# Optimization experiments

Hardware: AMD Instinct MI355X
Metric: run time of the kernel (lower is better)

## Reference

```python
import jax, jax.numpy as jnp
import numpy as np
from jax import lax

# ---- static config (ProposalLayer config object) ----
BASE_SIZE = 16
RATIOS = np.array([0.5, 1.0, 2.0])
SCALES = np.array([8.0, 16.0, 32.0])
STRIDE = 16
PRE_NMS_TOPN = 6000
POST_NMS_TOPN = 300
MIN_THRESHOLD = 16.0
NMS_THRESH = 0.7
IMG_W = 4096
IMG_H = 2048
NEG_INF = jnp.float32(-1e30)


def _generate_anchors(base_size, ratios, scales):
    w = h = float(base_size)
    x_ctr = y_ctr = 0.5 * (base_size - 1)
    size = w * h
    size_ratios = size / ratios
    ws = np.round(np.sqrt(size_ratios))          # (R,)
    hs = np.round(ws * ratios)                   # (R,)
    ws = (ws[:, None] * scales[None, :]).ravel() # (R*S,)
    hs = (hs[:, None] * scales[None, :]).ravel()
    anchors = np.stack([x_ctr - 0.5 * (ws - 1), y_ctr - 0.5 * (hs - 1),
                        x_ctr + 0.5 * (ws - 1), y_ctr + 0.5 * (hs - 1)], axis=1)
    return anchors.astype(np.float32)            # (A, 4) in x1,y1,x2,y2


def _all_anchors(height, width, stride):
    anchors = _generate_anchors(BASE_SIZE, RATIOS, SCALES)      # (A,4)
    sx = np.arange(width) * stride
    sy = np.arange(height) * stride
    mx, my = np.meshgrid(sx, sy)                                # (H,W) each
    shifts = np.stack([mx.ravel(), my.ravel(), mx.ravel(), my.ravel()], axis=1)
    shifts = shifts.reshape(-1, 1, 4).astype(np.float32)        # (K,1,4), K iterates h-major
    return (anchors[None] + shifts).reshape(-1, 4)              # (K*A, 4)


def _decode(deltas, anchors):
    # deltas: (B, N, 4); anchors: (N, 4) -> boxes (B, N, 4)
    aw = anchors[:, 2] - anchors[:, 0] + 1.0
    ah = anchors[:, 3] - anchors[:, 1] + 1.0
    acx = anchors[:, 0] + 0.5 * (aw - 1.0)
    acy = anchors[:, 1] + 0.5 * (ah - 1.0)
    dx, dy, dw, dh = deltas[..., 0], deltas[..., 1], deltas[..., 2], deltas[..., 3]
    pcx = dx * aw + acx
    pcy = dy * ah + acy
    pw = jnp.exp(dw) * aw
    ph = jnp.exp(dh) * ah
    return jnp.stack([pcx - 0.5 * pw, pcy - 0.5 * ph,
                      pcx + 0.5 * pw, pcy + 0.5 * ph], axis=-1)


def _nms_single(boxes, scores):
    # boxes (N,4), scores (N,) -> greedy NMS, fixed POST_NMS_TOPN outputs
    areas = (boxes[:, 2] - boxes[:, 0] + 1.0) * (boxes[:, 3] - boxes[:, 1] + 1.0)

    def body(live, _):
        i = jnp.argmax(live)
        box = boxes[i]
        sc = scores[i]
        xx1 = jnp.maximum(box[0], boxes[:, 0])
        yy1 = jnp.maximum(box[1], boxes[:, 1])
        xx2 = jnp.minimum(box[2], boxes[:, 2])
        yy2 = jnp.minimum(box[3], boxes[:, 3])
        inter = jnp.maximum(xx2 - xx1 + 1.0, 0.0) * jnp.maximum(yy2 - yy1 + 1.0, 0.0)
        iou = inter / (areas[i] + areas - inter)
        live = jnp.where(iou > NMS_THRESH, NEG_INF, live)
        live = live.at[i].set(NEG_INF)
        return live, (box, sc)

    _, (out_boxes, out_scores) = lax.scan(body, scores, None, length=POST_NMS_TOPN)
    return out_boxes, out_scores  # (P,4), (P,)


def reference(labels_pred, bbox_reg):
    B = labels_pred.shape[0]
    H, W = labels_pred.shape[-2:]
    anchors = jnp.asarray(_all_anchors(H, W, STRIDE))           # (K*A,4)

    # objectness score = fg channel after (B,2A,H,W)->(B,H,W,2A)->(B,KA,2)
    scores = jnp.transpose(labels_pred, (0, 2, 3, 1)).reshape(B, -1, 2)[..., 1]
    deltas = jnp.transpose(bbox_reg, (0, 2, 3, 1)).reshape(B, -1, 4)

    boxes = _decode(deltas, anchors)                            # (B,KA,4)
    x = jnp.clip(boxes[..., 0::2], 0.0, IMG_W - 1.0)
    y = jnp.clip(boxes[..., 1::2], 0.0, IMG_H - 1.0)
    boxes = jnp.stack([x[..., 0], y[..., 0], x[..., 1], y[..., 1]], axis=-1)

    keep = ((boxes[..., 2] - boxes[..., 0] + 1.0 >= MIN_THRESHOLD) &
            (boxes[..., 3] - boxes[..., 1] + 1.0 >= MIN_THRESHOLD))
    masked = jnp.where(keep, scores, NEG_INF)

    # pre-NMS top-k of kept anchors by score (assumes keep.sum >= PRE_NMS_TOPN)
    top_scores_masked, idx = lax.top_k(masked, PRE_NMS_TOPN)    # (B,P)
    top_scores = jnp.take_along_axis(scores, idx, axis=1)
    top_boxes = jnp.take_along_axis(boxes, idx[..., None], axis=1)

    out_boxes, out_scores = jax.vmap(_nms_single)(top_boxes, top_scores)
    return out_boxes, out_scores


def setup_inputs() -> dict:
    key = jax.random.key(0)
    k1, k2 = jax.random.split(key)
    labels_pred = jax.random.normal(k1, (16, 18, 128, 256), dtype=jnp.float32)
    bbox_reg = jax.random.normal(k2, (16, 36, 128, 256), dtype=jnp.float32)
    return {"labels_pred": labels_pred, "bbox_reg": bbox_reg}
```

## Files before the change

### kernel.cpp

```cpp
#include <hip/hip_runtime.h>
#include <stdint.h>

#define NBATCH 16
#define NANCH  9
#define NHGT   128
#define NWID   256
#define NHW    (NHGT * NWID)
#define NTOT   (NHW * NANCH)
#define PRE    6000
#define POST   300
#define CAPN   8192
#define BINS   8192
#define BIN_SHIFT 19
#define NWORDS 94
#define NWSTRIDE 96
#define RROWS  384
#define JQ     1536

#define MIDP 0x1.6666668p-1

__device__ __constant__ float c_AW[NANCH] = {184.f,368.f,736.f,128.f,256.f,512.f,88.f,176.f,352.f};
__device__ __constant__ float c_AH[NANCH] = {96.f,192.f,384.f,128.f,256.f,512.f,176.f,352.f,704.f};

__device__ __forceinline__ uint32_t f2key(float f) {
    uint32_t u = __float_as_uint(f);
    return (u & 0x80000000u) ? ~u : (u | 0x80000000u);
}

__device__ __forceinline__ bool iou_sup(const float4 bi, float areaI, const float4 bj, float areaJ) {
    float xx1 = fmaxf(bi.x, bj.x);
    float yy1 = fmaxf(bi.y, bj.y);
    float xx2 = fminf(bi.z, bj.z);
    float yy2 = fminf(bi.w, bj.w);
    float iw = fmaxf(__fadd_rn(__fsub_rn(xx2, xx1), 1.f), 0.f);
    float ih = fmaxf(__fadd_rn(__fsub_rn(yy2, yy1), 1.f), 0.f);
    float inter = __fmul_rn(iw, ih);
    float uni = __fsub_rn(__fadd_rn(areaI, areaJ), inter);
    return ((double)inter >= (double)uni * MIDP);
}

__device__ __forceinline__ bool decode_clip(float dx, float dy, float dw, float dh,
                                            float aw, float ah, float acx, float acy,
                                            float& x1, float& y1, float& x2, float& y2) {
    float pcx = __fadd_rn(__fmul_rn(dx, aw), acx);
    float pcy = __fadd_rn(__fmul_rn(dy, ah), acy);
    float pw  = __fmul_rn(expf(dw), aw);
    float ph  = __fmul_rn(expf(dh), ah);
    float hx  = __fmul_rn(0.5f, pw);
    float hy  = __fmul_rn(0.5f, ph);
    x1 = __fsub_rn(pcx, hx);
    y1 = __fsub_rn(pcy, hy);
    x2 = __fadd_rn(pcx, hx);
    y2 = __fadd_rn(pcy, hy);
    x1 = fminf(fmaxf(x1, 0.f), 4095.f);
    x2 = fminf(fmaxf(x2, 0.f), 4095.f);
    y1 = fminf(fmaxf(y1, 0.f), 2047.f);
    y2 = fminf(fmaxf(y2, 0.f), 2047.f);
    float wpl = __fadd_rn(__fsub_rn(x2, x1), 1.f);
    float hpl = __fadd_rn(__fsub_rn(y2, y1), 1.f);
    return (wpl >= 16.f) && (hpl >= 16.f);
}

__global__ __launch_bounds__(256) void k_zero(uint4* __restrict__ ghist4,
                                              uint32_t* __restrict__ cntthr) {
    int g = blockIdx.x * 256 + threadIdx.x;
    if (blockIdx.x < 128) {
        ghist4[g] = make_uint4(0, 0, 0, 0);
    } else {
        if (threadIdx.x < 32) cntthr[threadIdx.x] = 0;
    }
}

__global__ __launch_bounds__(256) void k_hist(const float* __restrict__ lab,
                                              const float* __restrict__ reg,
                                              uint32_t* __restrict__ ghist,
                                              uint32_t* __restrict__ keys) {
    __shared__ uint32_t hist[BINS];
    for (int i = threadIdx.x; i < BINS; i += 256) hist[i] = 0;
    __syncthreads();
    int b = blockIdx.x >> 5, sub = blockIdx.x & 31;
    int hw = (sub << 10) | (threadIdx.x << 2);
    int h = hw >> 8, w = hw & 255;
    const float* lb = lab + (size_t)b * 18 * NHW + hw;
    const float* rb = reg + (size_t)b * 36 * NHW + hw;
    uint32_t* kb = keys + (size_t)b * NANCH * NHW + hw;
    float acy  = (float)(h * 16) + 7.5f;
    float acx0 = (float)(w * 16) + 7.5f;
    float acx1 = acx0 + 16.0f;
    float acx2 = acx0 + 32.0f;
    float acx3 = acx0 + 48.0f;
#pragma unroll
    for (int a = 0; a < NANCH; ++a) {
        float4 s  = *(const float4*)&lb[(2 * a + 1) * NHW];
        float4 dx = *(const float4*)&rb[(4 * a + 0) * NHW];
        float4 dy = *(const float4*)&rb[(4 * a + 1) * NHW];
        float4 dwv = *(const float4*)&rb[(4 * a + 2) * NHW];
        float4 dhv = *(const float4*)&rb[(4 * a + 3) * NHW];
        float x1, y1, x2, y2;
        bool k0 = decode_clip(dx.x, dy.x, dwv.x, dhv.x, c_AW[a], c_AH[a], acx0, acy, x1, y1, x2, y2);
        bool k1 = decode_clip(dx.y, dy.y, dwv.y, dhv.y, c_AW[a], c_AH[a], acx1, acy, x1, y1, x2, y2);
        bool k2 = decode_clip(dx.z, dy.z, dwv.z, dhv.z, c_AW[a], c_AH[a], acx2, acy, x1, y1, x2, y2);
        bool k3 = decode_clip(dx.w, dy.w, dwv.w, dhv.w, c_AW[a], c_AH[a], acx3, acy, x1, y1, x2, y2);
        uint32_t key0 = f2key(k0 ? s.x : -1e30f);
        uint32_t key1 = f2key(k1 ? s.y : -1e30f);
        uint32_t key2 = f2key(k2 ? s.z : -1e30f);
        uint32_t key3 = f2key(k3 ? s.w : -1e30f);
        *(uint4*)&kb[a * NHW] = make_uint4(key0, key1, key2, key3);
        atomicAdd(&hist[key0 >> BIN_SHIFT], 1u);
        atomicAdd(&hist[key1 >> BIN_SHIFT], 1u);
        atomicAdd(&hist[key2 >> BIN_SHIFT], 1u);
        atomicAdd(&hist[key3 >> BIN_SHIFT], 1u);
    }
    __syncthreads();
    uint32_t* gh = ghist + ((size_t)b << 13);
    for (int i = threadIdx.x; i < BINS; i += 256) {
        uint32_t c = hist[i];
        if (c) atomicAdd(&gh[i], c);
    }
}

__global__ __launch_bounds__(256) void k_thresh(const uint32_t* __restrict__ ghist,
                                                uint32_t* __restrict__ thresh) {
    __shared__ uint32_t part[256];
    int b = blockIdx.x;
    const uint32_t* gh = ghist + ((size_t)b << 13);
    uint32_t p = 0;
    int base = threadIdx.x * 32;
    for (int k = 0; k < 32; ++k) p += gh[base + k];
    part[threadIdx.x] = p;
    __syncthreads();
    if (threadIdx.x == 0) {
        uint32_t cum = 0;
        int tb = 0;
        for (int c = 255; c >= 0; --c) {
            if (cum + part[c] >= (uint32_t)PRE) {
                for (int i = 31; i >= 0; --i) {
                    cum += gh[c * 32 + i];
                    if (cum >= (uint32_t)PRE) { tb = c * 32 + i; break; }
                }
                break;
            }
            cum += part[c];
        }
        thresh[b] = (uint32_t)tb << BIN_SHIFT;
    }
}

__global__ __launch_bounds__(256) void k_compact(const uint32_t* __restrict__ keys,
                                                 const uint32_t* __restrict__ thresh,
                                                 uint32_t* __restrict__ cnt,
                                                 uint64_t* __restrict__ cand) {
    __shared__ uint64_t stage[2304];
    __shared__ uint32_t sCount;
    __shared__ uint32_t sBase;
    if (threadIdx.x == 0) sCount = 0;
    __syncthreads();
    int bid = blockIdx.x;
    int b = bid >> 7;
    int hw = ((bid & 127) << 8) | threadIdx.x;
    int lane = threadIdx.x & 63;
    const uint32_t* kb = keys + (size_t)b * NANCH * NHW + hw;
    uint32_t th = thresh[b];
#pragma unroll
    for (int a = 0; a < NANCH; ++a) {
        uint32_t key = kb[a * NHW];
        bool valid = (key >= th);
        uint64_t mask = __ballot(valid);
        if (mask) {
            int leader = __ffsll((unsigned long long)mask) - 1;
            uint32_t wb = 0;
            if (lane == leader) wb = atomicAdd(&sCount, (uint32_t)__popcll(mask));
            wb = (uint32_t)__shfl((int)wb, leader);
            if (valid) {
                int rank = __popcll(mask & ((1ull << lane) - 1ull));
                uint32_t n = (uint32_t)(hw * NANCH + a);
                stage[wb + rank] = ((uint64_t)key << 32) | (uint32_t)(~n);
            }
        }
    }
    __syncthreads();
    if (threadIdx.x == 0) sBase = atomicAdd(&cnt[b], sCount);
    __syncthreads();
    uint32_t total = sCount, base = sBase;
    for (uint32_t i = threadIdx.x; i < total; i += 256) {
        uint32_t pos = base + i;
        if (pos < (uint32_t)CAPN) cand[(size_t)b * CAPN + pos] = stage[i];
    }
}

__global__ __launch_bounds__(512) void k_sortA(const uint32_t* __restrict__ cnt,
                                               uint64_t* __restrict__ cand) {
    __shared__ uint64_t sm[1024];
    int b = blockIdx.x >> 3, c = blockIdx.x & 7;
    uint32_t C = cnt[b];
    if (C > (uint32_t)CAPN) C = CAPN;
    uint64_t* cb = cand + (size_t)b * CAPN;
    int base = c << 10;
    for (int li = threadIdx.x; li < 1024; li += 512) {
        int gi = base + li;
        sm[li] = (gi < (int)C) ? cb[gi] : 0ull;
    }
    __syncthreads();
    for (int k = 2; k <= 1024; k <<= 1) {
        for (int j = k >> 1; j > 0; j >>= 1) {
            for (int li = threadIdx.x; li < 1024; li += 512) {
                int lxj = li ^ j;
                if (lxj > li) {
                    uint64_t va = sm[li], vb = sm[lxj];
                    bool up = ((li & k) == 0);
                    bool sw = up ? (va < vb) : (va > vb);
                    if (sw) { sm[li] = vb; sm[lxj] = va; }
                }
            }
            __syncthreads();
        }
    }
    for (int li = threadIdx.x; li < 1024; li += 512) cb[base + li] = sm[li];
}

__global__ __launch_bounds__(256) void k_merge(const uint64_t* __restrict__ src,
                                               uint64_t* __restrict__ dst,
                                               int Rlog) {
    int g = blockIdx.x * 256 + threadIdx.x;
    if (g >= NBATCH * CAPN) return;
    int b = g >> 13;
    int p = g & (CAPN - 1);
    int R = 1 << Rlog;
    int pair = p >> (Rlog + 1);
    int q = p & ((R << 1) - 1);
    const uint64_t* A = src + (size_t)b * CAPN + ((size_t)(pair << 1) << Rlog);
    const uint64_t* B = A + R;
    int lo = (q > R) ? (q - R) : 0;
    int hi = (q < R) ? q : R;
    while (lo < hi) {
        int mid = (lo + hi) >> 1;
        if (A[mid] > B[q - mid - 1]) lo = mid + 1; else hi = mid;
    }
    int i = lo, j = q - lo;
    uint64_t aV = (i < R) ? A[i] : 0ull;
    uint64_t bV = (j < R) ? B[j] : 0ull;
    dst[(size_t)b * CAPN + p] = (aV > bV) ? aV : bV;
}

__global__ __launch_bounds__(256) void k_mergegather(const uint64_t* __restrict__ cand,
                                                     const float* __restrict__ lab,
                                                     const float* __restrict__ reg,
                                                     float4* __restrict__ boxes,
                                                     float* __restrict__ scores) {
    int g = blockIdx.x * 256 + threadIdx.x;
    if (g >= NBATCH * PRE) return;
    int b = g / PRE, p = g - b * PRE;
    const uint64_t* A = cand + (size_t)b * CAPN;
    const uint64_t* B = A + 4096;
    int lo = (p > 4096) ? (p - 4096) : 0;
    int hi = (p < 4096) ? p : 4096;
    while (lo < hi) {
        int mid = (lo + hi) >> 1;
        if (A[mid] > B[p - mid - 1]) lo = mid + 1; else hi = mid;
    }
    int i = lo, j = p - lo;
    uint64_t aV = (i < 4096) ? A[i] : 0ull;
    uint64_t bV = (j < 4096) ? B[j] : 0ull;
    uint64_t v = (aV > bV) ? aV : bV;
    uint32_t n = ~(uint32_t)(v & 0xFFFFFFFFull);
    if (n >= (uint32_t)NTOT) n = 0;
    int a = (int)(n % NANCH);
    int hw = (int)(n / NANCH);
    int w = hw & 255, h = hw >> 8;
    const float* lb0 = lab + (size_t)b * 18 * NHW;
    const float* rb0 = reg + (size_t)b * 36 * NHW;
    float s  = lb0[(2 * a + 1) * NHW + hw];
    float dx = rb0[(4 * a + 0) * NHW + hw];
    float dy = rb0[(4 * a + 1) * NHW + hw];
    float dwv = rb0[(4 * a + 2) * NHW + hw];
    float dhv = rb0[(4 * a + 3) * NHW + hw];
    float acx = (float)(w * 16) + 7.5f;
    float acy = (float)(h * 16) + 7.5f;
    float x1, y1, x2, y2;
    decode_clip(dx, dy, dwv, dhv, c_AW[a], c_AH[a], acx, acy, x1, y1, x2, y2);
    boxes[b * PRE + p] = make_float4(x1, y1, x2, y2);
    scores[b * PRE + p] = s;
}

__global__ __launch_bounds__(512) void k_iou(const float4* __restrict__ boxes,
                                             uint64_t* __restrict__ supp) {
    __shared__ float4 lb[JQ];
    __shared__ float  la[JQ];
    int quad = blockIdx.x & 3;
    int rblk = (blockIdx.x >> 2) & 15;
    int b    = blockIdx.x >> 6;
    const float4* bb = boxes + b * PRE;
    int jbase  = quad * JQ;
    int jcount = (quad == 3) ? (PRE - 3 * JQ) : JQ;
    for (int i = threadIdx.x; i < jcount; i += 512) {
        float4 v = bb[jbase + i];
        lb[i] = v;
        la[i] = __fmul_rn(__fadd_rn(__fsub_rn(v.z, v.x), 1.f),
                          __fadd_rn(__fsub_rn(v.w, v.y), 1.f));
    }
    __syncthreads();
    int wave = threadIdx.x >> 6, lane = threadIdx.x & 63;
    int wlo = quad * 24;
    int whi = (quad == 3) ? NWORDS : (wlo + 24);
    int r0 = rblk + 16 * wave;
    int r1 = r0 + 128;
    int r2 = r0 + 256;
    float4 bi0 = bb[r0];
    float4 bi1 = bb[r1];
    float4 bi2 = bb[r2];
    float a0 = __fmul_rn(__fadd_rn(__fsub_rn(bi0.z, bi0.x), 1.f),
                         __fadd_rn(__fsub_rn(bi0.w, bi0.y), 1.f));
    float a1 = __fmul_rn(__fadd_rn(__fsub_rn(bi1.z, bi1.x), 1.f),
                         __fadd_rn(__fsub_rn(bi1.w, bi1.y), 1.f));
    float a2 = __fmul_rn(__fadd_rn(__fsub_rn(bi2.z, bi2.x), 1.f),
                         __fadd_rn(__fsub_rn(bi2.w, bi2.y), 1.f));
    uint64_t keep0 = 0ull, keep1 = 0ull, keep2 = 0ull;
    int w0 = r0 >> 6;
    int wstart = (wlo > w0) ? wlo : w0;
    for (int w = wstart; w < whi; ++w) {
        int j = (w << 6) | lane;
        bool s0 = false, s1 = false, s2 = false;
        if (j < PRE) {
            int idx = j - jbase;
            float4 bj = lb[idx];
            float aj = la[idx];
            s0 = iou_sup(bi0, a0, bj, aj);
            s1 = iou_sup(bi1, a1, bj, aj);
            s2 = iou_sup(bi2, a2, bj, aj);
        }
        uint64_t m0 = __ballot(s0);
        uint64_t m1 = __ballot(s1);
        uint64_t m2 = __ballot(s2);
        if (lane == w - wlo) { keep0 = m0; keep1 = m1; keep2 = m2; }
    }
    uint64_t* sr0 = supp + ((size_t)b * RROWS + r0) * NWSTRIDE;
    uint64_t* sr1 = supp + ((size_t)b * RROWS + r1) * NWSTRIDE;
    uint64_t* sr2 = supp + ((size_t)b * RROWS + r2) * NWSTRIDE;
    if (lane < 24) {
        uint64_t k0 = keep0, k1 = keep1, k2 = keep2;
        if (quad == 3 && lane >= 22) { k0 = 0; k1 = 0; k2 = 0; }
        sr0[wlo + lane] = k0;
        sr1[wlo + lane] = k1;
        sr2[wlo + lane] = k2;
    }
}

#define RD32(V, L) __builtin_amdgcn_readlane((uint32_t)(V), (L))
#define RDL64(V, L) ((uint64_t)(uint32_t)RD32((V), (L)) | \
                     ((uint64_t)(uint32_t)RD32((uint32_t)((V) >> 32), (L)) << 32))

#define LOADW(I) do {                                                           \
    const uint64_t* _rp = sbase + (size_t)(((I) << 6) + lane) * NWSTRIDE;       \
    m##I##0 = _rp[0]; m##I##1 = _rp[1]; m##I##2 = _rp[2];                       \
    m##I##3 = _rp[3]; m##I##4 = _rp[4]; m##I##5 = _rp[5];                       \
} while (0)

#define WINDOW(I) {                                                             \
    uint64_t curw = s##I;                                                       \
    while (curw) {                                                              \
        int rl = __ffsll((unsigned long long)curw) - 1;                         \
        if (lane == 0) idxb[t] = (uint32_t)(((I) << 6) + rl);                   \
        ++t;                                                                    \
        s0 &= ~RDL64(m##I##0, rl); s1 &= ~RDL64(m##I##1, rl);                   \
        s2 &= ~RDL64(m##I##2, rl); s3 &= ~RDL64(m##I##3, rl);                   \
        s4 &= ~RDL64(m##I##4, rl); s5 &= ~RDL64(m##I##5, rl);                   \
        if (t >= POST) { flag = 0; goto walk_done; }                            \
        curw = s##I;                                                            \
    }                                                                           \
}

__global__ __launch_bounds__(64, 1) void k_walk(const uint64_t* __restrict__ supp,
                                                uint32_t* __restrict__ flags,
                                                uint32_t* __restrict__ tsave,
                                                uint32_t* __restrict__ idxAll) {
    int b = blockIdx.x;
    int lane = threadIdx.x;
    uint32_t* idxb = idxAll + b * POST;
    const uint64_t* sbase = supp + (size_t)b * RROWS * NWSTRIDE;
    uint64_t m00,m01,m02,m03,m04,m05;
    uint64_t m10,m11,m12,m13,m14,m15;
    uint64_t m20,m21,m22,m23,m24,m25;
    uint64_t m30,m31,m32,m33,m34,m35;
    uint64_t m40,m41,m42,m43,m44,m45;
    uint64_t m50,m51,m52,m53,m54,m55;
    LOADW(0); LOADW(1); LOADW(2); LOADW(3); LOADW(4); LOADW(5);
    uint64_t s0 = ~0ull, s1 = ~0ull, s2 = ~0ull, s3 = ~0ull, s4 = ~0ull, s5 = ~0ull;
    int t = 0;
    int flag = 1;
    WINDOW(0)
    WINDOW(1)
    WINDOW(2)
    WINDOW(3)
    WINDOW(4)
    WINDOW(5)
    if (lane == 0) tsave[b] = (uint32_t)t;
walk_done:
    if (lane == 0) flags[b] = (uint32_t)flag;
}

__global__ __launch_bounds__(512) void k_resume(const float4* __restrict__ boxes,
                                                const uint64_t* __restrict__ supp,
                                                const uint32_t* __restrict__ flags,
                                                const uint32_t* __restrict__ tsave,
                                                uint32_t* __restrict__ idxAll) {
    int b = blockIdx.x;
    if (flags[b] == 0) return;
    __shared__ uint64_t alive[NWORDS];
    __shared__ uint32_t sCur;
    int tid = threadIdx.x;
    const float4* bb = boxes + b * PRE;
    uint32_t* idxb = idxAll + b * POST;
    if (tid < NWORDS) alive[tid] = (tid == NWORDS - 1) ? ((1ull << 48) - 1ull) : ~0ull;
    __syncthreads();
    int t0 = (int)tsave[b];
    for (int tt = 0; tt < t0; ++tt) {
        uint32_t r = idxb[tt];
        if (tid < NWORDS)
            alive[tid] &= ~supp[((size_t)b * RROWS + r) * NWSTRIDE + tid];
    }
    __syncthreads();
    for (int t = t0; t < POST; ++t) {
        if (tid == 0) sCur = 0xFFFFFFFFu;
        __syncthreads();
        if (tid < NWORDS) {
            uint64_t wd = alive[tid];
            if (wd) atomicMin(&sCur, (uint32_t)(tid * 64 + (__ffsll((unsigned long long)wd) - 1)));
        }
        __syncthreads();
        uint32_t cur = sCur;
        uint32_t e = (cur < (uint32_t)PRE) ? cur : 0u;
        if (tid == 0) {
            idxb[t] = e;
            if (cur < (uint32_t)PRE)
                atomicAnd(&alive[cur >> 6], ~(1ull << (cur & 63)));
        }
        if (cur < (uint32_t)PRE) {
            float4 bc = bb[e];
            float areaC = __fmul_rn(__fadd_rn(__fsub_rn(bc.z, bc.x), 1.f),
                                    __fadd_rn(__fsub_rn(bc.w, bc.y), 1.f));
            for (uint32_t j = cur + 1 + tid; j < (uint32_t)PRE; j += 512) {
                uint64_t wd = alive[j >> 6];
                if ((wd >> (j & 63)) & 1ull) {
                    float4 bj = bb[j];
                    float areaJ = __fmul_rn(__fadd_rn(__fsub_rn(bj.z, bj.x), 1.f),
                                            __fadd_rn(__fsub_rn(bj.w, bj.y), 1.f));
                    if (iou_sup(bc, areaC, bj, areaJ))
                        atomicAnd(&alive[j >> 6], ~(1ull << (j & 63)));
                }
            }
        }
        __syncthreads();
    }
}

__global__ __launch_bounds__(256) void k_out(const float4* __restrict__ boxes,
                                             const float* __restrict__ scores,
                                             const uint32_t* __restrict__ idxAll,
                                             float* __restrict__ out) {
    int g = blockIdx.x * 256 + threadIdx.x;
    if (g >= NBATCH * POST) return;
    int b = g / POST;
    uint32_t i = idxAll[g];
    if (i >= (uint32_t)PRE) i = 0;
    float4 bc = boxes[b * PRE + i];
    size_t ob = (size_t)g * 4;
    out[ob + 0] = bc.x; out[ob + 1] = bc.y;
    out[ob + 2] = bc.z; out[ob + 3] = bc.w;
    out[(size_t)NBATCH * POST * 4 + g] = scores[b * PRE + i];
}

extern "C" void kernel_launch(void* const* d_in, const int* in_sizes, int n_in,
                              void* d_out, int out_size, void* d_ws, size_t ws_size,
                              hipStream_t stream) {
    (void)in_sizes; (void)n_in; (void)out_size; (void)ws_size;
    const float* lab = (const float*)d_in[0];
    const float* reg = (const float*)d_in[1];
    float* out = (float*)d_out;
    char* ws = (char*)d_ws;

    uint32_t* ghist  = (uint32_t*)(ws + 0);
    uint32_t* cnt    = (uint32_t*)(ws + 524288);
    uint32_t* thr    = (uint32_t*)(ws + 524352);
    uint64_t* cand   = (uint64_t*)(ws + 524416);
    float4*   boxes  = (float4*)  (ws + 1572992);
    float*    scores = (float*)   (ws + 3108992);
    uint64_t* supp   = (uint64_t*)(ws + 3492992);
    uint32_t* flags  = (uint32_t*)(ws + 8211584);
    uint32_t* tsave  = (uint32_t*)(ws + 8211648);
    uint32_t* idx    = (uint32_t*)(ws + 8211712);
    uint32_t* keys   = (uint32_t*)(ws + 8230912);
    uint64_t* cand2  = (uint64_t*)(ws + 27105280);

    k_zero       <<<129, 256, 0, stream>>>((uint4*)ghist, cnt);
    k_hist       <<<512, 256, 0, stream>>>(lab, reg, ghist, keys);
    k_thresh     <<<NBATCH, 256, 0, stream>>>(ghist, thr);
    k_compact    <<<2048, 256, 0, stream>>>(keys, thr, cnt, cand);
    k_sortA      <<<NBATCH * 8, 512, 0, stream>>>(cnt, cand);
    k_merge      <<<NBATCH * CAPN / 256, 256, 0, stream>>>(cand, cand2, 10);
    k_merge      <<<NBATCH * CAPN / 256, 256, 0, stream>>>(cand2, cand, 11);
    k_mergegather<<<(NBATCH * PRE + 255) / 256, 256, 0, stream>>>(cand, lab, reg, boxes, scores);
    k_iou        <<<NBATCH * 64, 512, 0, stream>>>(boxes, supp);
    k_walk       <<<NBATCH, 64, 0, stream>>>(supp, flags, tsave, idx);
    k_resume     <<<NBATCH, 512, 0, stream>>>(boxes, supp, flags, tsave, idx);
    k_out        <<<(NBATCH * POST + 255) / 256, 256, 0, stream>>>(boxes, scores, idx, out);
}
```

Baseline: 175.3 us.

## Limit IoU suppression matrix to top-384 block and restart fallback from scratch

The IoU kernel now computes suppression bits only among the top 384 boxes (384x384) instead of 384 rows against all 6000 candidates. This shrinks both the pairwise IoU work and the matrix written to memory. The bitmask walk already read only those columns, so it is unchanged. If the walk cannot reach 300 keeps, the resume kernel now reruns greedy NMS from the beginning rather than continuing from the saved state. That fallback becomes more expensive when it triggers.

Result: faster. 152.7 us (-12.9%).

```diff
diff --git a/kernel.cpp b/kernel.cpp
--- a/kernel.cpp
+++ b/kernel.cpp
@@ -13,9 +13,8 @@
 #define BINS   8192
 #define BIN_SHIFT 19
 #define NWORDS 94
-#define NWSTRIDE 96
 #define RROWS  384
-#define JQ     1536
+#define SWORDS 6
 
 #define MIDP 0x1.6666668p-1
 
@@ -284,64 +283,29 @@
 
 __global__ __launch_bounds__(512) void k_iou(const float4* __restrict__ boxes,
                                              uint64_t* __restrict__ supp) {
-    __shared__ float4 lb[JQ];
-    __shared__ float  la[JQ];
-    int quad = blockIdx.x & 3;
-    int rblk = (blockIdx.x >> 2) & 15;
-    int b    = blockIdx.x >> 6;
+    __shared__ float4 lb[RROWS];
+    __shared__ float  la[RROWS];
+    int blk = blockIdx.x % 48;
+    int b   = blockIdx.x / 48;
     const float4* bb = boxes + b * PRE;
-    int jbase  = quad * JQ;
-    int jcount = (quad == 3) ? (PRE - 3 * JQ) : JQ;
-    for (int i = threadIdx.x; i < jcount; i += 512) {
-        float4 v = bb[jbase + i];
+    for (int i = threadIdx.x; i < RROWS; i += 512) {
+        float4 v = bb[i];
         lb[i] = v;
         la[i] = __fmul_rn(__fadd_rn(__fsub_rn(v.z, v.x), 1.f),
                           __fadd_rn(__fsub_rn(v.w, v.y), 1.f));
     }
     __syncthreads();
     int wave = threadIdx.x >> 6, lane = threadIdx.x & 63;
-    int wlo = quad * 24;
-    int whi = (quad == 3) ? NWORDS : (wlo + 24);
-    int r0 = rblk + 16 * wave;
-    int r1 = r0 + 128;
-    int r2 = r0 + 256;
-    float4 bi0 = bb[r0];
-    float4 bi1 = bb[r1];
-    float4 bi2 = bb[r2];
-    float a0 = __fmul_rn(__fadd_rn(__fsub_rn(bi0.z, bi0.x), 1.f),
-                         __fadd_rn(__fsub_rn(bi0.w, bi0.y), 1.f));
-    float a1 = __fmul_rn(__fadd_rn(__fsub_rn(bi1.z, bi1.x), 1.f),
-                         __fadd_rn(__fsub_rn(bi1.w, bi1.y), 1.f));
-    float a2 = __fmul_rn(__fadd_rn(__fsub_rn(bi2.z, bi2.x), 1.f),
-                         __fadd_rn(__fsub_rn(bi2.w, bi2.y), 1.f));
-    uint64_t keep0 = 0ull, keep1 = 0ull, keep2 = 0ull;
-    int w0 = r0 >> 6;
-    int wstart = (wlo > w0) ? wlo : w0;
-    for (int w = wstart; w < whi; ++w) {
+    int r = (blk << 3) + wave;
+    float4 bi = lb[r];
+    float ai = la[r];
+    uint64_t* sr = supp + ((size_t)b * RROWS + r) * SWORDS;
+#pragma unroll
+    for (int w = 0; w < SWORDS; ++w) {
         int j = (w << 6) | lane;
-        bool s0 = false, s1 = false, s2 = false;
-        if (j < PRE) {
-            int idx = j - jbase;
-            float4 bj = lb[idx];
-            float aj = la[idx];
-            s0 = iou_sup(bi0, a0, bj, aj);
-            s1 = iou_sup(bi1, a1, bj, aj);
-            s2 = iou_sup(bi2, a2, bj, aj);
-        }
-        uint64_t m0 = __ballot(s0);
-        uint64_t m1 = __ballot(s1);
-        uint64_t m2 = __ballot(s2);
-        if (lane == w - wlo) { keep0 = m0; keep1 = m1; keep2 = m2; }
-    }
-    uint64_t* sr0 = supp + ((size_t)b * RROWS + r0) * NWSTRIDE;
-    uint64_t* sr1 = supp + ((size_t)b * RROWS + r1) * NWSTRIDE;
-    uint64_t* sr2 = supp + ((size_t)b * RROWS + r2) * NWSTRIDE;
-    if (lane < 24) {
-        uint64_t k0 = keep0, k1 = keep1, k2 = keep2;
-        if (quad == 3 && lane >= 22) { k0 = 0; k1 = 0; k2 = 0; }
-        sr0[wlo + lane] = k0;
-        sr1[wlo + lane] = k1;
-        sr2[wlo + lane] = k2;
+        bool s = iou_sup(bi, ai, lb[j], la[j]);
+        uint64_t m = __ballot(s);
+        if (lane == 0) sr[w] = m;
     }
 }
 
@@ -350,7 +314,7 @@
                      ((uint64_t)(uint32_t)RD32((uint32_t)((V) >> 32), (L)) << 32))
 
 #define LOADW(I) do {                                                           \
-    const uint64_t* _rp = sbase + (size_t)(((I) << 6) + lane) * NWSTRIDE;       \
+    const uint64_t* _rp = sbase + (size_t)(((I) << 6) + lane) * SWORDS;         \
     m##I##0 = _rp[0]; m##I##1 = _rp[1]; m##I##2 = _rp[2];                       \
     m##I##3 = _rp[3]; m##I##4 = _rp[4]; m##I##5 = _rp[5];                       \
 } while (0)
@@ -371,12 +335,11 @@
 
 __global__ __launch_bounds__(64, 1) void k_walk(const uint64_t* __restrict__ supp,
                                                 uint32_t* __restrict__ flags,
-                                                uint32_t* __restrict__ tsave,
                                                 uint32_t* __restrict__ idxAll) {
     int b = blockIdx.x;
     int lane = threadIdx.x;
     uint32_t* idxb = idxAll + b * POST;
-    const uint64_t* sbase = supp + (size_t)b * RROWS * NWSTRIDE;
+    const uint64_t* sbase = supp + (size_t)b * RROWS * SWORDS;
     uint64_t m00,m01,m02,m03,m04,m05;
     uint64_t m10,m11,m12,m13,m14,m15;
     uint64_t m20,m21,m22,m23,m24,m25;
@@ -393,15 +356,12 @@
     WINDOW(3)
     WINDOW(4)
     WINDOW(5)
-    if (lane == 0) tsave[b] = (uint32_t)t;
 walk_done:
     if (lane == 0) flags[b] = (uint32_t)flag;
 }
 
 __global__ __launch_bounds__(512) void k_resume(const float4* __restrict__ boxes,
-                                                const uint64_t* __restrict__ supp,
                                                 const uint32_t* __restrict__ flags,
-                                                const uint32_t* __restrict__ tsave,
                                                 uint32_t* __restrict__ idxAll) {
     int b = blockIdx.x;
     if (flags[b] == 0) return;
@@ -412,14 +372,7 @@
     uint32_t* idxb = idxAll + b * POST;
     if (tid < NWORDS) alive[tid] = (tid == NWORDS - 1) ? ((1ull << 48) - 1ull) : ~0ull;
     __syncthreads();
-    int t0 = (int)tsave[b];
-    for (int tt = 0; tt < t0; ++tt) {
-        uint32_t r = idxb[tt];
-        if (tid < NWORDS)
-            alive[tid] &= ~supp[((size_t)b * RROWS + r) * NWSTRIDE + tid];
-    }
-    __syncthreads();
-    for (int t = t0; t < POST; ++t) {
+    for (int t = 0; t < POST; ++t) {
         if (tid == 0) sCur = 0xFFFFFFFFu;
         __syncthreads();
         if (tid < NWORDS) {
@@ -485,11 +438,10 @@
     float4*   boxes  = (float4*)  (ws + 1572992);
     float*    scores = (float*)   (ws + 3108992);
     uint64_t* supp   = (uint64_t*)(ws + 3492992);
-    uint32_t* flags  = (uint32_t*)(ws + 8211584);
-    uint32_t* tsave  = (uint32_t*)(ws + 8211648);
-    uint32_t* idx    = (uint32_t*)(ws + 8211712);
-    uint32_t* keys   = (uint32_t*)(ws + 8230912);
-    uint64_t* cand2  = (uint64_t*)(ws + 27105280);
+    uint32_t* flags  = (uint32_t*)(ws + 3787904);
+    uint32_t* idx    = (uint32_t*)(ws + 3787968);
+    uint32_t* keys   = (uint32_t*)(ws + 3807168);
+    uint64_t* cand2  = (uint64_t*)(ws + 22681536);
 
     k_zero       <<<129, 256, 0, stream>>>((uint4*)ghist, cnt);
     k_hist       <<<512, 256, 0, stream>>>(lab, reg, ghist, keys);
@@ -499,8 +451,8 @@
     k_merge      <<<NBATCH * CAPN / 256, 256, 0, stream>>>(cand, cand2, 10);
     k_merge      <<<NBATCH * CAPN / 256, 256, 0, stream>>>(cand2, cand, 11);
     k_mergegather<<<(NBATCH * PRE + 255) / 256, 256, 0, stream>>>(cand, lab, reg, boxes, scores);
-    k_iou        <<<NBATCH * 64, 512, 0, stream>>>(boxes, supp);
-    k_walk       <<<NBATCH, 64, 0, stream>>>(supp, flags, tsave, idx);
-    k_resume     <<<NBATCH, 512, 0, stream>>>(boxes, supp, flags, tsave, idx);
+    k_iou        <<<NBATCH * 48, 512, 0, stream>>>(boxes, supp);
+    k_walk       <<<NBATCH, 64, 0, stream>>>(supp, flags, idx);
+    k_resume     <<<NBATCH, 512, 0, stream>>>(boxes, flags, idx);
     k_out        <<<(NBATCH * POST + 255) / 256, 256, 0, stream>>>(boxes, scores, idx, out);
 }
```
